# Performance work log

Hardware: AMD Instinct MI355X
Metric: run time of the kernel (lower is better)

The kernel has to match this reference:

```python
import jax, jax.numpy as jnp
import numpy as np

N_QUBITS = 8
EMBED_DIM = 1024
FFN_DIM = 4096


def setup_inputs() -> dict:
    key = jax.random.key(0)
    ks = jax.random.split(key, 6)
    x = jax.random.normal(ks[0], (8, 4096, EMBED_DIM), dtype=jnp.float32)
    # trainable RY rotation angles, one per wire (torchquantum RY has_params=True)
    theta = jax.random.normal(ks[1], (N_QUBITS,), dtype=jnp.float32)
    # torch nn.Linear params: W [out, in], b [out]
    W1 = jax.random.normal(ks[2], (FFN_DIM, N_QUBITS), dtype=jnp.float32) / np.sqrt(N_QUBITS)
    b1 = jnp.zeros((FFN_DIM,), dtype=jnp.float32)
    W2 = jax.random.normal(ks[3], (EMBED_DIM, FFN_DIM), dtype=jnp.float32) / np.sqrt(FFN_DIM)
    b2 = jnp.zeros((EMBED_DIM,), dtype=jnp.float32)
    return {"x": x, "theta": theta, "W1": W1, "b1": b1, "W2": W2, "b2": b2}


def reference(x, theta, W1, b1, W2, b2):
    # Quantum layer: per token, encoder resets state to |0..0>, applies RX(x_i)
    # on wire i, then trainable RY(theta_i), then measures <Z_i>. The circuit has
    # no entangling gates, so it factorizes per wire with the closed form:
    #   <Z_i> = cos(theta_i) * cos(x[..., i])
    # (RY(t)RX(a)|0> gives <Z> = cos t * cos a). Vectorized over batch and seq.
    q = jnp.cos(theta) * jnp.cos(x[..., :N_QUBITS])   # [B, S, n_qubits]
    # dropout is identity in eval mode
    h = jax.nn.relu(jnp.einsum('bsq,fq->bsf', q, W1) + b1)  # [B, S, ffn]
    out = jnp.einsum('bsf,ef->bse', h, W2) + b2              # [B, S, embed]
    return out
```

## Files before the change

### kernel.cpp

```cpp
#include <hip/hip_runtime.h>
#include <cstdint>
#include <cstddef>


#define M_TOT 32768L
#define N_DIM 1024
#define K_DIM 4096
#define BM 256
#define BN 256
#define BK 64
#define NT_K (K_DIM / BK)
#define CM_MAX 16384L

typedef __attribute__((ext_vector_type(8))) short short8;
typedef __attribute__((ext_vector_type(4))) float f32x4;

__device__ __forceinline__ uint16_t f2bf(float f) {
  uint32_t u = __builtin_bit_cast(uint32_t, f);
  uint32_t r = (u + 0x7fffu + ((u >> 16) & 1u)) >> 16;
  return (uint16_t)r;
}

__device__ __forceinline__ void gload_lds16(const void* gsrc, void* ldst) {
  __builtin_amdgcn_global_load_lds(
      (const __attribute__((address_space(1))) void*)gsrc,
      (__attribute__((address_space(3))) void*)ldst, 16, 0, 0);
}

__global__ __launch_bounds__(256) void prep_w2(const float* __restrict__ W2,
                                               uint16_t* __restrict__ W2sw) {
  long idx = (long)blockIdx.x * 256 + threadIdx.x;
  long e8 = idx * 8;
  int e = (int)(e8 >> 12);
  int k = (int)(e8 & 4095);
  float4 v0 = *(const float4*)(W2 + e8);
  float4 v1 = *(const float4*)(W2 + e8 + 4);
  union { uint16_t u[8]; uint4 v; } pk;
  pk.u[0] = f2bf(v0.x); pk.u[1] = f2bf(v0.y); pk.u[2] = f2bf(v0.z); pk.u[3] = f2bf(v0.w);
  pk.u[4] = f2bf(v1.x); pk.u[5] = f2bf(v1.y); pk.u[6] = f2bf(v1.z); pk.u[7] = f2bf(v1.w);
  int sg = ((k >> 3) & 7) ^ (e & 7);
  uint16_t* dst = W2sw + (long)e * 4096 + (k & ~63) + sg * 8;
  *(uint4*)dst = pk.v;
}

__global__ __launch_bounds__(256) void h_kernel(const float* __restrict__ x,
                                                const float* __restrict__ theta,
                                                const float* __restrict__ W1,
                                                const float* __restrict__ b1,
                                                uint16_t* __restrict__ Hsw) {
  __shared__ float qs[64][8];
  int tid = threadIdx.x;
  long m0 = (long)blockIdx.x * 64;
  int f = blockIdx.y * 256 + tid;

  for (int idx = tid; idx < 512; idx += 256) {
    int t = idx >> 3, i = idx & 7;
    qs[t][i] = __cosf(theta[i]) * cosf(x[(m0 + t) * 1024 + i]);
  }
  __syncthreads();

  const float4* w1p = (const float4*)(W1 + (long)f * 8);
  float4 wa = w1p[0];
  float4 wb = w1p[1];
  float bb = b1[f];
  int fblk = f & ~63;
  int grp = (f >> 3) & 7;
  int fw = f & 7;

#pragma unroll 4
  for (int t = 0; t < 64; ++t) {
    long m = m0 + t;
    const float* q = qs[t];
    float h = bb;
    h += q[0] * wa.x + q[1] * wa.y + q[2] * wa.z + q[3] * wa.w;
    h += q[4] * wb.x + q[5] * wb.y + q[6] * wb.z + q[7] * wb.w;
    h = fmaxf(h, 0.0f);
    int sg = grp ^ ((int)m & 7);
    Hsw[m * K_DIM + fblk + sg * 8 + fw] = f2bf(h);
  }
}

__global__ __launch_bounds__(512, 2) void gemm_kernel(const uint16_t* __restrict__ Hsw,
                                                      const uint16_t* __restrict__ W2sw,
                                                      const float* __restrict__ b2,
                                                      float* __restrict__ out) {
  __shared__ uint16_t LA[2 * BM * BK];
  __shared__ uint16_t LB[2 * BN * BK];

  int nwg = gridDim.x;
  int bid = blockIdx.x;
  int sw = bid;
  if ((nwg & 7) == 0) { int cpx = nwg >> 3; sw = (bid & 7) * cpx + (bid >> 3); }
  const int NTN = N_DIM / BN;
  int mt = sw / NTN;
  int nt = sw - mt * NTN;
  long m0 = (long)mt * BM;
  int n0 = nt * BN;

  int tid = threadIdx.x;
  int lane = tid & 63;
  int wave_m = (tid >> 6) >> 2;
  int wave_n = (tid >> 6) & 3;
  int wmB = wave_m * 128;
  int wnB = wave_n * 64;

  int r  = lane & 15;
  int kq = lane >> 4;
  int xr = r & 7;

  int rowS = tid >> 3;
  int colS = (tid & 7) * 8;
  const uint16_t* srcA = Hsw  + (m0 + rowS) * K_DIM + colS;
  const uint16_t* srcB = W2sw + ((long)(n0 + rowS)) * K_DIM + colS;
  int ldsWB = (tid & ~63) * 8;

#define STAGE_A(p, h, j, t) \
  gload_lds16(srcA + (long)((h)*128 + (j)*64) * K_DIM + (t)*BK, \
              &LA[(p)*16384 + ((h)*128 + (j)*64)*BK + ldsWB])
#define STAGE_B(p, h, j, t) \
  gload_lds16(srcB + (long)((h)*128 + (j)*64) * K_DIM + (t)*BK, \
              &LB[(p)*16384 + ((h)*128 + (j)*64)*BK + ldsWB])

#define BAR() do { asm volatile("" ::: "memory"); __builtin_amdgcn_s_barrier(); \
                   asm volatile("" ::: "memory"); } while (0)

#define LDA_F(p, mf_, ks_) \
  (*(const short8*)&LA[(p)*16384 + (wmB + (mf_)*16 + r)*BK + ((((ks_)*4 + kq) ^ xr)*8)])
#define LDB_F(p, nf_, ks_) \
  (*(const short8*)&LB[(p)*16384 + (wnB + (nf_)*16 + r)*BK + ((((ks_)*4 + kq) ^ xr)*8)])

#define MFMA_PHASE(mh, nh) do { \
    __builtin_amdgcn_s_setprio(1); \
    _Pragma("unroll") for (int i_ = 0; i_ < 4; ++i_) \
    _Pragma("unroll") for (int j_ = 0; j_ < 2; ++j_) \
    _Pragma("unroll") for (int ks_ = 0; ks_ < 2; ++ks_) \
      acc[(mh)*4 + i_][(nh)*2 + j_] = __builtin_amdgcn_mfma_f32_16x16x32_bf16( \
          a[i_][ks_], bq[(nh)][j_][ks_], acc[(mh)*4 + i_][(nh)*2 + j_], 0, 0, 0); \
    __builtin_amdgcn_s_setprio(0); \
  } while (0)

  f32x4 acc[8][4];
#pragma unroll
  for (int i = 0; i < 8; ++i)
#pragma unroll
    for (int j = 0; j < 4; ++j) acc[i][j] = (f32x4){0.f, 0.f, 0.f, 0.f};

  short8 a[4][2];
  short8 bq[2][2][2];

#pragma unroll
  for (int h = 0; h < 2; ++h)
#pragma unroll
    for (int j = 0; j < 2; ++j) STAGE_A(0, h, j, 0);
#pragma unroll
  for (int h = 0; h < 2; ++h)
#pragma unroll
    for (int j = 0; j < 2; ++j) STAGE_B(0, h, j, 0);
#pragma unroll
  for (int h = 0; h < 2; ++h)
#pragma unroll
    for (int j = 0; j < 2; ++j) STAGE_A(1, h, j, 1);
#pragma unroll
  for (int h = 0; h < 2; ++h)
#pragma unroll
    for (int j = 0; j < 2; ++j) STAGE_B(1, h, j, 1);
  asm volatile("s_waitcnt vmcnt(8)" ::: "memory");
  BAR();

#pragma unroll 2
  for (int u = 0; u < NT_K; ++u) {
    int p = u & 1;
    bool st = (u < NT_K - 2);

#pragma unroll
    for (int i = 0; i < 4; ++i)
#pragma unroll
      for (int ks = 0; ks < 2; ++ks) a[i][ks] = LDA_F(p, i, ks);
#pragma unroll
    for (int j = 0; j < 2; ++j)
#pragma unroll
      for (int ks = 0; ks < 2; ++ks) bq[0][j][ks] = LDB_F(p, j, ks);
    MFMA_PHASE(0, 0);
#pragma unroll
    for (int j = 0; j < 2; ++j)
#pragma unroll
      for (int ks = 0; ks < 2; ++ks) bq[1][j][ks] = LDB_F(p, 2 + j, ks);
    BAR();

    MFMA_PHASE(0, 1);
#pragma unroll
    for (int i = 0; i < 4; ++i)
#pragma unroll
      for (int ks = 0; ks < 2; ++ks) a[i][ks] = LDA_F(p, 4 + i, ks);
    if (st) { STAGE_A(p, 0, 0, u + 2); STAGE_A(p, 1, 0, u + 2); }
    BAR();

    MFMA_PHASE(1, 1);
    if (st) { STAGE_B(p, 0, 0, u + 2); STAGE_B(p, 0, 1, u + 2); }
    BAR();

    MFMA_PHASE(1, 0);
    if (st)                 { asm volatile("s_waitcnt vmcnt(4)" ::: "memory"); }
    else if (u == NT_K - 2) { asm volatile("s_waitcnt vmcnt(0)" ::: "memory"); }
    if (st) { STAGE_A(p, 0, 1, u + 2); STAGE_A(p, 1, 1, u + 2);
              STAGE_B(p, 1, 0, u + 2); STAGE_B(p, 1, 1, u + 2); }
    BAR();
  }

  float bb[4];
#pragma unroll
  for (int nf = 0; nf < 4; ++nf) bb[nf] = b2[n0 + wnB + nf * 16 + r];
  long mbase = m0 + wmB + kq * 4;
#pragma unroll
  for (int mf = 0; mf < 8; ++mf) {
#pragma unroll
    for (int nf = 0; nf < 4; ++nf) {
      int n = n0 + wnB + nf * 16 + r;
#pragma unroll
      for (int rg = 0; rg < 4; ++rg) {
        out[(mbase + mf * 16 + rg) * N_DIM + n] = acc[mf][nf][rg] + bb[nf];
      }
    }
  }
#undef STAGE_A
#undef STAGE_B
#undef BAR
#undef LDA_F
#undef LDB_F
#undef MFMA_PHASE
}

extern "C" void kernel_launch(void* const* d_in, const int* in_sizes, int n_in,
                              void* d_out, int out_size, void* d_ws, size_t ws_size,
                              hipStream_t stream) {
  const float* x     = (const float*)d_in[0];
  const float* theta = (const float*)d_in[1];
  const float* W1    = (const float*)d_in[2];
  const float* b1    = (const float*)d_in[3];
  const float* W2    = (const float*)d_in[4];
  const float* b2    = (const float*)d_in[5];
  float* out = (float*)d_out;

  const size_t W2SW_BYTES = (size_t)N_DIM * K_DIM * 2;
  uint16_t* W2sw = (uint16_t*)d_ws;
  uint16_t* Hsw  = (uint16_t*)((char*)d_ws + W2SW_BYTES);

  size_t avail = ws_size > W2SW_BYTES ? ws_size - W2SW_BYTES : 0;
  long CM = (long)(avail / ((size_t)K_DIM * 2));
  CM &= ~255L;
  if (CM > CM_MAX) CM = CM_MAX;
  if (CM < 256) CM = 256;

  prep_w2<<<2048, 256, 0, stream>>>(W2, W2sw);

  for (long m0 = 0; m0 < M_TOT; m0 += CM) {
    long mc = M_TOT - m0;
    if (mc > CM) mc = CM;
    dim3 gA((unsigned)(mc / 64), K_DIM / 256);
    h_kernel<<<gA, 256, 0, stream>>>(x + m0 * N_DIM, theta, W1, b1, Hsw);
    unsigned ngb = (unsigned)((mc / BM) * (N_DIM / BN));
    gemm_kernel<<<ngb, 512, 0, stream>>>(Hsw, W2sw, b2, out + m0 * N_DIM);
  }
}
```

Baseline: 313.7 us.

## Vectorize H-kernel stores and software-pipeline LDS fragment loads in GEMM

The h_kernel now has each thread compute 8 consecutive FFN outputs per token and write them as a single 16-byte store, with the grid's y-dimension shrunk to match. The goal is fewer scattered 2-byte global writes. The GEMM main loop is restructured with separate a0/a1 and b0/b1 register sets, so the next tile's first A/B fragments are read from LDS during the last MFMA quarter of the current tile. This overlaps LDS reads with MFMA work at the cost of more VGPRs, and it changes the order of global->LDS staging and vmcnt waits, which risks races or lower occupancy.

```diff
diff --git a/kernel.cpp b/kernel.cpp
--- a/kernel.cpp
+++ b/kernel.cpp
@@ -51,7 +51,8 @@
   __shared__ float qs[64][8];
   int tid = threadIdx.x;
   long m0 = (long)blockIdx.x * 64;
-  int f = blockIdx.y * 256 + tid;
+  int g = blockIdx.y * 256 + tid;
+  int f0 = g * 8;
 
   for (int idx = tid; idx < 512; idx += 256) {
     int t = idx >> 3, i = idx & 7;
@@ -59,24 +60,35 @@
   }
   __syncthreads();
 
-  const float4* w1p = (const float4*)(W1 + (long)f * 8);
-  float4 wa = w1p[0];
-  float4 wb = w1p[1];
-  float bb = b1[f];
-  int fblk = f & ~63;
-  int grp = (f >> 3) & 7;
-  int fw = f & 7;
-
-#pragma unroll 4
+  float4 w[16];
+#pragma unroll
+  for (int j = 0; j < 8; ++j) {
+    w[2 * j]     = *(const float4*)(W1 + (long)(f0 + j) * 8);
+    w[2 * j + 1] = *(const float4*)(W1 + (long)(f0 + j) * 8 + 4);
+  }
+  float bb[8];
+#pragma unroll
+  for (int j = 0; j < 8; ++j) bb[j] = b1[f0 + j];
+
+  int blk = (g >> 3) * 64;
+  int gw = g & 7;
+
+#pragma unroll 2
   for (int t = 0; t < 64; ++t) {
     long m = m0 + t;
-    const float* q = qs[t];
-    float h = bb;
-    h += q[0] * wa.x + q[1] * wa.y + q[2] * wa.z + q[3] * wa.w;
-    h += q[4] * wb.x + q[5] * wb.y + q[6] * wb.z + q[7] * wb.w;
-    h = fmaxf(h, 0.0f);
-    int sg = grp ^ ((int)m & 7);
-    Hsw[m * K_DIM + fblk + sg * 8 + fw] = f2bf(h);
+    float q0 = qs[t][0], q1 = qs[t][1], q2 = qs[t][2], q3 = qs[t][3];
+    float q4 = qs[t][4], q5 = qs[t][5], q6 = qs[t][6], q7 = qs[t][7];
+    union { uint16_t u[8]; uint4 v; } pk;
+#pragma unroll
+    for (int j = 0; j < 8; ++j) {
+      float h = bb[j];
+      h += q0 * w[2 * j].x + q1 * w[2 * j].y + q2 * w[2 * j].z + q3 * w[2 * j].w;
+      h += q4 * w[2 * j + 1].x + q5 * w[2 * j + 1].y + q6 * w[2 * j + 1].z + q7 * w[2 * j + 1].w;
+      h = fmaxf(h, 0.0f);
+      pk.u[j] = f2bf(h);
+    }
+    int sg = gw ^ ((int)m & 7);
+    *(uint4*)&Hsw[m * K_DIM + blk + sg * 8] = pk.v;
   }
 }
 
@@ -129,13 +141,13 @@
 #define LDB_F(p, nf_, ks_) \
   (*(const short8*)&LB[(p)*16384 + (wnB + (nf_)*16 + r)*BK + ((((ks_)*4 + kq) ^ xr)*8)])
 
-#define MFMA_PHASE(mh, nh) do { \
+#define MFMA_Q(AARR, BARR, mh, nh) do { \
     __builtin_amdgcn_s_setprio(1); \
     _Pragma("unroll") for (int i_ = 0; i_ < 4; ++i_) \
     _Pragma("unroll") for (int j_ = 0; j_ < 2; ++j_) \
     _Pragma("unroll") for (int ks_ = 0; ks_ < 2; ++ks_) \
       acc[(mh)*4 + i_][(nh)*2 + j_] = __builtin_amdgcn_mfma_f32_16x16x32_bf16( \
-          a[i_][ks_], bq[(nh)][j_][ks_], acc[(mh)*4 + i_][(nh)*2 + j_], 0, 0, 0); \
+          AARR[i_][ks_], BARR[j_][ks_], acc[(mh)*4 + i_][(nh)*2 + j_], 0, 0, 0); \
     __builtin_amdgcn_s_setprio(0); \
   } while (0)
 
@@ -145,8 +157,10 @@
 #pragma unroll
     for (int j = 0; j < 4; ++j) acc[i][j] = (f32x4){0.f, 0.f, 0.f, 0.f};
 
-  short8 a[4][2];
-  short8 bq[2][2][2];
+  short8 a0[4][2];
+  short8 a1[4][2];
+  short8 b0[2][2];
+  short8 b1v[2][2];
 
 #pragma unroll
   for (int h = 0; h < 2; ++h)
@@ -166,44 +180,55 @@
     for (int j = 0; j < 2; ++j) STAGE_B(1, h, j, 1);
   asm volatile("s_waitcnt vmcnt(8)" ::: "memory");
   BAR();
+#pragma unroll
+  for (int i = 0; i < 4; ++i)
+#pragma unroll
+    for (int ks = 0; ks < 2; ++ks) a0[i][ks] = LDA_F(0, i, ks);
+#pragma unroll
+  for (int j = 0; j < 2; ++j)
+#pragma unroll
+    for (int ks = 0; ks < 2; ++ks) b0[j][ks] = LDB_F(0, j, ks);
 
 #pragma unroll 2
   for (int u = 0; u < NT_K; ++u) {
     int p = u & 1;
     bool st = (u < NT_K - 2);
-
+    bool rd = (u < NT_K - 1);
+
+    MFMA_Q(a0, b0, 0, 0);
+#pragma unroll
+    for (int j = 0; j < 2; ++j)
+#pragma unroll
+      for (int ks = 0; ks < 2; ++ks) b1v[j][ks] = LDB_F(p, 2 + j, ks);
 #pragma unroll
     for (int i = 0; i < 4; ++i)
 #pragma unroll
-      for (int ks = 0; ks < 2; ++ks) a[i][ks] = LDA_F(p, i, ks);
-#pragma unroll
-    for (int j = 0; j < 2; ++j)
-#pragma unroll
-      for (int ks = 0; ks < 2; ++ks) bq[0][j][ks] = LDB_F(p, j, ks);
-    MFMA_PHASE(0, 0);
-#pragma unroll
-    for (int j = 0; j < 2; ++j)
-#pragma unroll
-      for (int ks = 0; ks < 2; ++ks) bq[1][j][ks] = LDB_F(p, 2 + j, ks);
-    BAR();
-
-    MFMA_PHASE(0, 1);
-#pragma unroll
-    for (int i = 0; i < 4; ++i)
-#pragma unroll
-      for (int ks = 0; ks < 2; ++ks) a[i][ks] = LDA_F(p, 4 + i, ks);
+      for (int ks = 0; ks < 2; ++ks) a1[i][ks] = LDA_F(p, 4 + i, ks);
+    BAR();
+
+    MFMA_Q(a0, b1v, 0, 1);
     if (st) { STAGE_A(p, 0, 0, u + 2); STAGE_A(p, 1, 0, u + 2); }
     BAR();
 
-    MFMA_PHASE(1, 1);
-    if (st) { STAGE_B(p, 0, 0, u + 2); STAGE_B(p, 0, 1, u + 2); }
-    BAR();
-
-    MFMA_PHASE(1, 0);
-    if (st)                 { asm volatile("s_waitcnt vmcnt(4)" ::: "memory"); }
+    MFMA_Q(a1, b1v, 1, 1);
+    if (st) { STAGE_B(p, 0, 0, u + 2); STAGE_B(p, 0, 1, u + 2);
+              STAGE_B(p, 1, 0, u + 2); STAGE_B(p, 1, 1, u + 2); }
+    if (st)                 { asm volatile("s_waitcnt vmcnt(6)" ::: "memory"); }
     else if (u == NT_K - 2) { asm volatile("s_waitcnt vmcnt(0)" ::: "memory"); }
-    if (st) { STAGE_A(p, 0, 1, u + 2); STAGE_A(p, 1, 1, u + 2);
-              STAGE_B(p, 1, 0, u + 2); STAGE_B(p, 1, 1, u + 2); }
+    BAR();
+
+    MFMA_Q(a1, b0, 1, 0);
+    if (rd) {
+#pragma unroll
+      for (int i = 0; i < 4; ++i)
+#pragma unroll
+        for (int ks = 0; ks < 2; ++ks) a0[i][ks] = LDA_F(p ^ 1, i, ks);
+#pragma unroll
+      for (int j = 0; j < 2; ++j)
+#pragma unroll
+        for (int ks = 0; ks < 2; ++ks) b0[j][ks] = LDB_F(p ^ 1, j, ks);
+    }
+    if (st) { STAGE_A(p, 0, 1, u + 2); STAGE_A(p, 1, 1, u + 2); }
     BAR();
   }
 
@@ -227,7 +252,7 @@
 #undef BAR
 #undef LDA_F
 #undef LDB_F
-#undef MFMA_PHASE
+#undef MFMA_Q
 }
 
 extern "C" void kernel_launch(void* const* d_in, const int* in_sizes, int n_in,
@@ -256,7 +281,7 @@
   for (long m0 = 0; m0 < M_TOT; m0 += CM) {
     long mc = M_TOT - m0;
     if (mc > CM) mc = CM;
-    dim3 gA((unsigned)(mc / 64), K_DIM / 256);
+    dim3 gA((unsigned)(mc / 64), 2);
     h_kernel<<<gA, 256, 0, stream>>>(x + m0 * N_DIM, theta, W1, b1, Hsw);
     unsigned ngb = (unsigned)((mc / BM) * (N_DIM / BN));
     gemm_kernel<<<ngb, 512, 0, stream>>>(Hsw, W2sw, b2, out + m0 * N_DIM);
```

After: 309.0 us. Within noise of the previous version (-1.5%).
